# Optimization experiments

Hardware: AMD Instinct MI355X
Metric: run time of the kernel (lower is better)

Reference implementation:

```python
import jax, jax.numpy as jnp
import numpy as np

EPS = 1e-5
DIM, QK, PDIM = 448, 16, 96

def _bn(y, w, b, rm, rv):
    # inference-mode BatchNorm2d over channel axis 1
    scale = (w / jnp.sqrt(rv + EPS))[None, :, None, None]
    return (y - rm[None, :, None, None]) * scale + b[None, :, None, None]

def setup_inputs() -> dict:
    key = jax.random.key(0)
    ks = jax.random.split(key, 13)
    B, H, W = 64, 32, 32
    return {
        "x": jax.random.normal(ks[0], (B, DIM, H, W), jnp.float32),
        "gn_w": jax.random.uniform(ks[1], (PDIM,), jnp.float32, 0.5, 1.5),
        "gn_b": 0.02 * jax.random.normal(ks[2], (PDIM,), jnp.float32),
        "qkv_w": jax.random.normal(ks[3], (2 * QK + PDIM, PDIM), jnp.float32) * (PDIM ** -0.5),
        "qkv_bn_w": jax.random.uniform(ks[4], (2 * QK + PDIM,), jnp.float32, 0.5, 1.5),
        "qkv_bn_b": 0.02 * jax.random.normal(ks[5], (2 * QK + PDIM,), jnp.float32),
        "qkv_bn_rm": 0.02 * jax.random.normal(ks[6], (2 * QK + PDIM,), jnp.float32),
        "qkv_bn_rv": jax.random.uniform(ks[7], (2 * QK + PDIM,), jnp.float32, 0.5, 1.5),
        "proj_w": jax.random.normal(ks[8], (DIM, DIM), jnp.float32) * (DIM ** -0.5),
        "proj_bn_w": jax.random.uniform(ks[9], (DIM,), jnp.float32, 0.5, 1.5),
        "proj_bn_b": 0.02 * jax.random.normal(ks[10], (DIM,), jnp.float32),
        "proj_bn_rm": 0.02 * jax.random.normal(ks[11], (DIM,), jnp.float32),
        "proj_bn_rv": jax.random.uniform(ks[12], (DIM,), jnp.float32, 0.5, 1.5),
    }

def reference(x, gn_w, gn_b, qkv_w, qkv_bn_w, qkv_bn_b, qkv_bn_rm, qkv_bn_rv,
              proj_w, proj_bn_w, proj_bn_b, proj_bn_rm, proj_bn_rv):
    B, C, H, W = x.shape
    scale = QK ** -0.5
    x1, x2 = x[:, :PDIM], x[:, PDIM:]
    # GroupNorm with num_groups=1: normalize over (C,H,W) per sample
    mu = jnp.mean(x1, axis=(1, 2, 3), keepdims=True)
    var = jnp.var(x1, axis=(1, 2, 3), keepdims=True)
    x1n = (x1 - mu) * jax.lax.rsqrt(var + EPS)
    x1n = x1n * gn_w[None, :, None, None] + gn_b[None, :, None, None]
    # 1x1 conv (no bias) + BN
    qkv = jnp.einsum('bchw,oc->bohw', x1n, qkv_w)
    qkv = _bn(qkv, qkv_bn_w, qkv_bn_b, qkv_bn_rm, qkv_bn_rv)
    q, k, v = qkv[:, :QK], qkv[:, QK:2 * QK], qkv[:, 2 * QK:]
    N = H * W
    q = q.reshape(B, QK, N); k = k.reshape(B, QK, N); v = v.reshape(B, PDIM, N)
    attn = jnp.einsum('bcn,bcm->bnm', q, k) * scale          # [B,N,N]
    attn = jax.nn.softmax(attn, axis=-1)
    x1o = jnp.einsum('bcm,bnm->bcn', v, attn).reshape(B, PDIM, H, W)
    y = jnp.concatenate([x1o, x2], axis=1)
    y = jax.nn.relu(y)
    y = jnp.einsum('bchw,oc->bohw', y, proj_w)
    return _bn(y, proj_bn_w, proj_bn_b, proj_bn_rm, proj_bn_rv)
```

## Files before the change

### kernel.cpp

```cpp
#include <hip/hip_runtime.h>
#include <hip/hip_bf16.h>

#define EPS 1e-5f

constexpr int BB   = 64;
constexpr int CDIM = 448;
constexpr int PD   = 96;
constexpr int QKD  = 16;
constexpr int QO   = 128;
constexpr int NPix = 1024;
constexpr int NCH  = 14;

constexpr size_t WS_MU  = 0;
constexpr size_t WS_RS  = 64;
constexpr size_t WS_QSC = 128;
constexpr size_t WS_QBI = 256;
constexpr size_t WS_PSC = 384;
constexpr size_t WS_PBI = 832;
constexpr size_t WS_WG  = 1280;
constexpr size_t WS_SWG = 13568;
constexpr size_t WS_WB  = 13696;
constexpr size_t WS_WGT = 13824;
constexpr size_t WS_WGH = 26112;
constexpr size_t WS_YB  = 32768;
constexpr size_t WS_W16 = WS_YB + (size_t)BB*NPix*CDIM/2;
constexpr size_t WS_QT  = WS_W16 + (size_t)512*CDIM/2;
constexpr size_t WS_KT  = WS_QT + (size_t)BB*NPix*32/2;
constexpr size_t WS_VB  = WS_KT + (size_t)BB*NPix*32/2;

typedef __attribute__((ext_vector_type(8))) short short8;
typedef __attribute__((ext_vector_type(8))) _Float16 half8;
typedef __attribute__((ext_vector_type(4))) float f32x4;

__device__ __forceinline__ unsigned short f2bf(float v) {
  __hip_bfloat16 h = __float2bfloat16(v);
  return *reinterpret_cast<unsigned short*>(&h);
}
__device__ __forceinline__ unsigned short f2h(float v) {
  _Float16 h = (_Float16)v;
  return *reinterpret_cast<unsigned short*>(&h);
}

typedef const __attribute__((address_space(1))) unsigned int* gp_t;
typedef __attribute__((address_space(3))) unsigned int* lp_t;
__device__ __forceinline__ void gload16(const void* g, void* l) {
  __builtin_amdgcn_global_load_lds((gp_t)g, (lp_t)l, 16, 0, 0);
}

constexpr int XT_BLOCKS = 11264;
constexpr int TAILB     = 209;
__global__ __launch_bounds__(256) void k_setup(
    const float* __restrict__ x,
    const float* __restrict__ gn_w, const float* __restrict__ gn_b,
    const float* __restrict__ qkv_w,
    const float* __restrict__ qbw, const float* __restrict__ qbb,
    const float* __restrict__ qbrm, const float* __restrict__ qbrv,
    const float* __restrict__ pw,
    const float* __restrict__ pbw, const float* __restrict__ pbb,
    const float* __restrict__ pbrm, const float* __restrict__ pbrv,
    float* __restrict__ ws, unsigned short* __restrict__ Wb,
    unsigned short* __restrict__ Ybc) {
  __shared__ float tile[32][65];
  float* red = &tile[0][0];
  int t = threadIdx.x;
  if (blockIdx.x >= TAILB) {
    int idx = blockIdx.x - TAILB;
    int nx = idx & 15, cy = (idx >> 4) % 11, b = idx / 176;
    int c0 = PD + cy * 32;
    int n0 = nx * 64;
#pragma unroll
    for (int i = 0; i < 2; ++i) {
      int k = t + i * 256;
      int c = k >> 4, q = k & 15;
      float4 v = reinterpret_cast<const float4*>(
                     x + ((size_t)b * CDIM + c0 + c) * NPix + n0)[q];
      *reinterpret_cast<float4*>(&tile[c][q * 4]) = v;
    }
    __syncthreads();
    int n = t >> 2, ch = t & 3;
    short8 o;
#pragma unroll
    for (int j = 0; j < 8; ++j)
      o[j] = (short)f2bf(fmaxf(tile[ch * 8 + j][n], 0.f));
    *reinterpret_cast<short8*>(
        &Ybc[(((size_t)b * NCH + 3 + cy) * NPix + n0 + n) * 32 + ch * 8]) = o;
    return;
  }
  int bid = blockIdx.x;
  if (bid < 64) {
    int b = bid;
    const float4* x4 = reinterpret_cast<const float4*>(x + (size_t)b * CDIM * NPix);
    float s = 0.f, ss = 0.f;
#pragma unroll 8
    for (int ii = 0; ii < PD * NPix / 4 / 256; ++ii) {
      float4 v = x4[t + ii * 256];
      s  += v.x + v.y + v.z + v.w;
      ss += v.x * v.x + v.y * v.y + v.z * v.z + v.w * v.w;
    }
#pragma unroll
    for (int o = 32; o > 0; o >>= 1) { s += __shfl_down(s, o); ss += __shfl_down(ss, o); }
    int wid = t >> 6;
    if ((t & 63) == 0) { red[wid] = s; red[4 + wid] = ss; }
    __syncthreads();
    if (t == 0) {
      float S  = red[0] + red[1] + red[2] + red[3];
      float SS = red[4] + red[5] + red[6] + red[7];
      const float inv_n = 1.f / (PD * NPix);
      float mu  = S * inv_n;
      float var = SS * inv_n - mu * mu;
      ws[WS_MU + b] = mu;
      ws[WS_RS + b] = rsqrtf(var + EPS);
    }
  } else if (bid < 96) {
    int o = (bid - 64) * 4 + (t >> 6);
    int lane = t & 63;
    unsigned short* Wgh = reinterpret_cast<unsigned short*>(ws + WS_WGH);
    float sw = 0.f, bb = 0.f;
    for (int c = lane; c < PD; c += 64) {
      float w  = qkv_w[o * PD + c];
      float wg = w * gn_w[c];
      Wgh[(size_t)o * PD + c] = f2h(wg);
      sw += wg;
      bb += w * gn_b[c];
    }
#pragma unroll
    for (int off = 32; off > 0; off >>= 1) {
      sw += __shfl_down(sw, off);
      bb += __shfl_down(bb, off);
    }
    if (lane == 0) {
      ws[WS_SWG + o] = sw;
      ws[WS_WB + o]  = bb;
      float sc = qbw[o] * rsqrtf(qbrv[o] + EPS);
      ws[WS_QSC + o] = sc;
      ws[WS_QBI + o] = qbb[o] - qbrm[o] * sc;
    }
  } else if (bid == 96) {
    for (int o = t; o < CDIM; o += 256) {
      float sc = pbw[o] * rsqrtf(pbrv[o] + EPS);
      ws[WS_PSC + o] = sc;
      ws[WS_PBI + o] = pbb[o] - pbrm[o] * sc;
    }
  } else {
    int idx = (bid - 97) * 256 + t;
    int row = idx / 56, sl = (idx % 56) * 8;
    short8 o = {};
    if (row < CDIM) {
      const float* src = pw + (size_t)row * CDIM + sl;
#pragma unroll
      for (int j = 0; j < 8; ++j) o[j] = (short)f2bf(src[j]);
    }
    *reinterpret_cast<short8*>(&Wb[(size_t)row * CDIM + sl]) = o;
  }
}

__global__ __launch_bounds__(256) void k_qkv2(const float* __restrict__ x,
                                              float* __restrict__ ws,
                                              unsigned short* __restrict__ qt,
                                              unsigned short* __restrict__ kt,
                                              unsigned short* __restrict__ vb) {
  __shared__ __align__(16) char smem[PD * 132 * 4];
  float*          xt = reinterpret_cast<float*>(smem);
  unsigned short* ld = reinterpret_cast<unsigned short*>(smem);

  int lin = blockIdx.x + 8 * blockIdx.y;
  int swz = (lin & 7) * 64 + (lin >> 3);
  int n0  = (swz & 7) * 128;
  int b   = swz >> 3;
  int t   = threadIdx.x;
  int lane = t & 63, w = t >> 6;
  int lo = lane & 15, hi = lane >> 4;

  const float4* xb4 = reinterpret_cast<const float4*>(x + (size_t)b * CDIM * NPix);
#pragma unroll
  for (int i = 0; i < 12; ++i) {
    int idx = t + i * 256;
    int row = idx >> 5, c4 = idx & 31;
    float4 v = xb4[row * (NPix / 4) + (n0 >> 2) + c4];
    *reinterpret_cast<float4*>(&xt[row * 132 + c4 * 4]) = v;
  }
  __syncthreads();

  const unsigned short* Wgh = reinterpret_cast<const unsigned short*>(ws + WS_WGH);
  f32x4 acc[8][2] = {{{}}};
#pragma unroll
  for (int kk = 0; kk < 3; ++kk) {
    half8 bfr[2];
#pragma unroll
    for (int nf = 0; nf < 2; ++nf) {
      int nr = w * 32 + nf * 16 + lo;
      half8 h;
#pragma unroll
      for (int j = 0; j < 8; ++j)
        h[j] = (_Float16)xt[(kk * 32 + hi * 8 + j) * 132 + nr];
      bfr[nf] = h;
    }
#pragma unroll
    for (int of = 0; of < 8; ++of) {
      half8 a = *reinterpret_cast<const half8*>(
          &Wgh[(size_t)(of * 16 + lo) * PD + kk * 32 + hi * 8]);
      acc[of][0] = __builtin_amdgcn_mfma_f32_16x16x32_f16(a, bfr[0], acc[of][0], 0, 0, 0);
      acc[of][1] = __builtin_amdgcn_mfma_f32_16x16x32_f16(a, bfr[1], acc[of][1], 0, 0, 0);
    }
  }
  float mu = ws[WS_MU + b], rs = ws[WS_RS + b];
  __syncthreads();
#pragma unroll
  for (int of = 0; of < 8; ++of) {
#pragma unroll
    for (int r = 0; r < 4; ++r) {
      int o = of * 16 + hi * 4 + r;
      float bias = ws[WS_WB + o] - rs * mu * ws[WS_SWG + o];
      float qs = ws[WS_QSC + o], qb = ws[WS_QBI + o];
      float postm = (o < QKD) ? 0.25f : 1.f;
#pragma unroll
      for (int nf = 0; nf < 2; ++nf) {
        int nl = w * 32 + nf * 16 + lo;
        float v = (qs * (rs * acc[of][nf][r] + bias) + qb) * postm;
        ld[o * 136 + nl] = f2h(v);
      }
    }
  }
  __syncthreads();
#pragma unroll
  for (int i = 0; i < 6; ++i) {
    int idx = t + i * 256;
    int row = idx >> 4, c8 = idx & 15;
    short8 v = *reinterpret_cast<const short8*>(&ld[(32 + row) * 136 + c8 * 8]);
    *reinterpret_cast<short8*>(&vb[((size_t)b * PD + row) * NPix + n0 + c8 * 8]) = v;
  }
#pragma unroll
  for (int i = 0; i < 4; ++i) {
    int idx = t + i * 256;
    int arr = idx >> 9;
    int rem = idx & 511;
    int n = rem >> 2, q4 = rem & 3;
    short8 o = {};
    if (q4 < 2) {
#pragma unroll
      for (int j = 0; j < 8; ++j)
        o[j] = (short)ld[(arr * 16 + q4 * 8 + j) * 136 + n];
    }
    unsigned short* dst = arr ? kt : qt;
    *reinterpret_cast<short8*>(&dst[((size_t)b * NPix + n0 + n) * 32 + q4 * 8]) = o;
  }
}

__global__ __launch_bounds__(512) void k_attn2(
    const unsigned short* __restrict__ qt,
    const unsigned short* __restrict__ kt,
    const unsigned short* __restrict__ vb,
    unsigned short* __restrict__ Ybc) {
  __shared__ __align__(16) unsigned short kt_s[128 * 40];
  __shared__ __align__(16) unsigned short vt_s[96 * 136];
  __shared__ __align__(16) unsigned short P_s[8 * 16 * 136];

  int lin = blockIdx.x + 8 * blockIdx.y;
  int swz = (lin & 7) * 64 + (lin >> 3);
  int n0  = (swz & 7) * 128;
  int b   = swz >> 3;
  int t  = threadIdx.x;
  int lane = t & 63, w = t >> 6;
  int lo = lane & 15, hi = lane >> 4;

  half8 q8 = *reinterpret_cast<const half8*>(
      &qt[((size_t)b * NPix + n0 + w * 16 + lo) * 32 + hi * 8]);

  const unsigned short* ktb = kt + (size_t)b * NPix * 32;
  const unsigned short* vbb = vb + (size_t)b * PD * NPix;

  f32x4 o[6] = {};
  float M = -1e30f, L = 0.f;
  f32x4 zero = {};

  for (int mt = 0; mt < 8; ++mt) {
    int m0 = mt * 128;
    int krow = t >> 2, kc4 = t & 3;
    float4 rk = *reinterpret_cast<const float4*>(&ktb[(size_t)(m0 + krow) * 32 + kc4 * 8]);
    float4 rv[3];
#pragma unroll
    for (int i = 0; i < 3; ++i) {
      int ci = t + 512 * i;
      int row = ci >> 4, c4 = ci & 15;
      rv[i] = *reinterpret_cast<const float4*>(&vbb[(size_t)row * NPix + m0 + c4 * 8]);
    }
    __syncthreads();
    *reinterpret_cast<float4*>(&kt_s[krow * 40 + kc4 * 8]) = rk;
#pragma unroll
    for (int i = 0; i < 3; ++i) {
      int ci = t + 512 * i;
      int row = ci >> 4, c4 = ci & 15;
      *reinterpret_cast<float4*>(&vt_s[row * 136 + c4 * 8]) = rv[i];
    }
    __syncthreads();

    f32x4 s[8];
    __builtin_amdgcn_s_setprio(1);
#pragma unroll
    for (int ss = 0; ss < 8; ++ss) {
      half8 a = *reinterpret_cast<const half8*>(&kt_s[(ss * 16 + lo) * 40 + hi * 8]);
      s[ss] = __builtin_amdgcn_mfma_f32_16x16x32_f16(a, q8, zero, 0, 0, 0);
    }
    __builtin_amdgcn_s_setprio(0);

    float tmax = s[0][0];
#pragma unroll
    for (int ss = 0; ss < 8; ++ss)
#pragma unroll
      for (int r = 0; r < 4; ++r) tmax = fmaxf(tmax, s[ss][r]);
    tmax = fmaxf(tmax, __shfl_xor(tmax, 16));
    tmax = fmaxf(tmax, __shfl_xor(tmax, 32));
    float newM = fmaxf(M, tmax);
    float fac = __expf(M - newM);
    M = newM;
    float psum = 0.f;
    unsigned pbase = (w * 16 + lo) * 136;
#pragma unroll
    for (int ss = 0; ss < 8; ++ss) {
      float p0 = __expf(s[ss][0] - M);
      float p1 = __expf(s[ss][1] - M);
      float p2 = __expf(s[ss][2] - M);
      float p3 = __expf(s[ss][3] - M);
      psum += (p0 + p1) + (p2 + p3);
      unsigned u01 = (unsigned)f2h(p0) | ((unsigned)f2h(p1) << 16);
      unsigned u23 = (unsigned)f2h(p2) | ((unsigned)f2h(p3) << 16);
      *reinterpret_cast<unsigned*>(&P_s[pbase + 16 * ss + 4 * hi])     = u01;
      *reinterpret_cast<unsigned*>(&P_s[pbase + 16 * ss + 4 * hi + 2]) = u23;
    }
    psum += __shfl_xor(psum, 16);
    psum += __shfl_xor(psum, 32);
    L = L * fac + psum;
#pragma unroll
    for (int cf = 0; cf < 6; ++cf)
#pragma unroll
      for (int r = 0; r < 4; ++r) o[cf][r] *= fac;
    asm volatile("s_waitcnt lgkmcnt(0)" ::: "memory");

    __builtin_amdgcn_s_setprio(1);
#pragma unroll
    for (int ks = 0; ks < 4; ++ks) {
      half8 pb = *reinterpret_cast<const half8*>(&P_s[pbase + ks * 32 + hi * 8]);
#pragma unroll
      for (int cf = 0; cf < 6; ++cf) {
        half8 va = *reinterpret_cast<const half8*>(&vt_s[(cf * 16 + lo) * 136 + ks * 32 + hi * 8]);
        o[cf] = __builtin_amdgcn_mfma_f32_16x16x32_f16(va, pb, o[cf], 0, 0, 0);
      }
    }
    __builtin_amdgcn_s_setprio(0);
  }

  float inv = 1.f / L;
  unsigned pbase = (w * 16 + lo) * 136;
#pragma unroll
  for (int cf = 0; cf < 6; ++cf) {
    float v0 = fmaxf(o[cf][0] * inv, 0.f);
    float v1 = fmaxf(o[cf][1] * inv, 0.f);
    float v2 = fmaxf(o[cf][2] * inv, 0.f);
    float v3 = fmaxf(o[cf][3] * inv, 0.f);
    unsigned u01 = (unsigned)f2bf(v0) | ((unsigned)f2bf(v1) << 16);
    unsigned u23 = (unsigned)f2bf(v2) | ((unsigned)f2bf(v3) << 16);
    *reinterpret_cast<unsigned*>(&P_s[pbase + cf * 16 + 4 * hi])     = u01;
    *reinterpret_cast<unsigned*>(&P_s[pbase + cf * 16 + 4 * hi + 2]) = u23;
  }
  asm volatile("s_waitcnt lgkmcnt(0)" ::: "memory");
#pragma unroll
  for (int j = 0; j < 3; ++j) {
    int k = lane + 64 * j;
    int n = k / 12, c8 = k % 12;
    short8 vv = *reinterpret_cast<const short8*>(&P_s[(w * 16 + n) * 136 + c8 * 8]);
    *reinterpret_cast<short8*>(
        &Ybc[(((size_t)b * NCH + (c8 >> 2)) * NPix + n0 + w * 16 + n) * 32
             + (c8 & 3) * 8]) = vv;
  }
}

__global__ __launch_bounds__(256) void k_projmm(
    const unsigned short* __restrict__ Wb,
    const unsigned short* __restrict__ Ybc,
    const float* __restrict__ ws,
    float* __restrict__ out) {
  __shared__ __align__(16) unsigned short At[3][128 * 32];
  int lin = blockIdx.x + 8 * (blockIdx.y + 4 * blockIdx.z);
  int swz = (lin & 7) * 256 + (lin >> 3);
  int m0  = (swz & 3) * 128;
  int n0  = ((swz >> 2) & 7) * 128;
  int b   = swz >> 5;
  int t  = threadIdx.x;
  int lane = t & 63, wid = t >> 6;
  int wm = wid >> 1, wn = wid & 1;
  int lo = lane & 15, hi = lane >> 4;

  const unsigned short* Arow = Wb + (size_t)m0 * CDIM;
  const unsigned short* Brow = Ybc + ((size_t)b * NCH * NPix + n0 + wn * 64) * 32;

  int chunk0 = wid * 128 + lane;
  int row0 = chunk0 >> 2, sl0 = (chunk0 & 3) ^ ((row0 >> 1) & 3);
  int chunk1 = chunk0 + 64;
  int row1 = chunk1 >> 2, sl1 = (chunk1 & 3) ^ ((row1 >> 1) & 3);

#define STAGE_A(bufi, s_)                                                      \
  do {                                                                         \
    gload16(Arow + (size_t)row0 * CDIM + (s_) * 32 + sl0 * 8,                  \
            &At[bufi][(wid * 128) * 8]);                                       \
    gload16(Arow + (size_t)row1 * CDIM + (s_) * 32 + sl1 * 8,                  \
            &At[bufi][(wid * 128 + 64) * 8]);                                  \
  } while (0)

#define LOADB(slot, s_)                                                        \
  do {                                                                         \
    _Pragma("unroll")                                                          \
    for (int f = 0; f < 4; ++f)                                                \
      bf[slot][f] = *reinterpret_cast<const short8*>(                          \
          &Brow[(size_t)(s_) * NPix * 32 + (f * 16 + lo) * 32 + hi * 8]);      \
  } while (0)

  short8 bf[2][4];
  f32x4 acc[4][4] = {{{}}};

  STAGE_A(0, 0);
  STAGE_A(1, 1);
  LOADB(0, 0);
  asm volatile("s_waitcnt vmcnt(6)" ::: "memory");
  __builtin_amdgcn_sched_barrier(0);
  __builtin_amdgcn_s_barrier();

#pragma unroll
  for (int s = 0; s < 14; ++s) {
    if (s + 2 <= 13) STAGE_A((s + 2) % 3, s + 2);
    if (s + 1 <= 13) LOADB((s + 1) & 1, s + 1);
    __builtin_amdgcn_sched_barrier(0);
    short8 af[4];
#pragma unroll
    for (int f = 0; f < 4; ++f) {
      int ar = wm * 64 + f * 16 + lo;
      int as = hi ^ ((ar >> 1) & 3);
      af[f] = *reinterpret_cast<const short8*>(&At[s % 3][ar * 32 + as * 8]);
    }
    asm volatile("s_waitcnt lgkmcnt(0)" ::: "memory");
    __builtin_amdgcn_sched_barrier(0);
#pragma unroll
    for (int i = 0; i < 4; ++i)
#pragma unroll
      for (int j = 0; j < 4; ++j)
        acc[i][j] = __builtin_amdgcn_mfma_f32_16x16x32_bf16(
            af[i], bf[s & 1][j], acc[i][j], 0, 0, 0);
    if (s < 13) {
      if (s <= 11) asm volatile("s_waitcnt vmcnt(6)" ::: "memory");
      else         asm volatile("s_waitcnt vmcnt(4)" ::: "memory");
      __builtin_amdgcn_sched_barrier(0);
      __builtin_amdgcn_s_barrier();
    }
  }
#undef STAGE_A
#undef LOADB

  int col = lane & 15, rq = lane >> 4;
#pragma unroll
  for (int i = 0; i < 4; ++i) {
    int ob = m0 + wm * 64 + i * 16 + rq * 4;
#pragma unroll
    for (int r = 0; r < 4; ++r) {
      int o = ob + r;
      if (o < CDIM) {
        float ps = ws[WS_PSC + o], pb = ws[WS_PBI + o];
        size_t base = ((size_t)b * CDIM + o) * NPix + n0 + wn * 64 + col;
#pragma unroll
        for (int j = 0; j < 4; ++j)
          out[base + j * 16] = ps * acc[i][j][r] + pb;
      }
    }
  }
}

extern "C" void kernel_launch(void* const* d_in, const int* in_sizes, int n_in,
                              void* d_out, int out_size, void* d_ws, size_t ws_size,
                              hipStream_t stream) {
  const float* x      = (const float*)d_in[0];
  const float* gn_w   = (const float*)d_in[1];
  const float* gn_b   = (const float*)d_in[2];
  const float* qkv_w  = (const float*)d_in[3];
  const float* qbw    = (const float*)d_in[4];
  const float* qbb    = (const float*)d_in[5];
  const float* qbrm   = (const float*)d_in[6];
  const float* qbrv   = (const float*)d_in[7];
  const float* pw     = (const float*)d_in[8];
  const float* pbw    = (const float*)d_in[9];
  const float* pbb    = (const float*)d_in[10];
  const float* pbrm   = (const float*)d_in[11];
  const float* pbrv   = (const float*)d_in[12];
  float* out = (float*)d_out;
  float* ws  = (float*)d_ws;
  unsigned short* Ybc = (unsigned short*)(ws + WS_YB);
  unsigned short* Wb  = (unsigned short*)(ws + WS_W16);
  unsigned short* qt  = (unsigned short*)(ws + WS_QT);
  unsigned short* kt  = (unsigned short*)(ws + WS_KT);
  unsigned short* vb  = (unsigned short*)(ws + WS_VB);

  k_setup<<<TAILB + XT_BLOCKS, 256, 0, stream>>>(
      x, gn_w, gn_b, qkv_w, qbw, qbb, qbrm, qbrv,
      pw, pbw, pbb, pbrm, pbrv, ws, Wb, Ybc);
  k_qkv2<<<dim3(8, BB), 256, 0, stream>>>(x, ws, qt, kt, vb);
  k_attn2<<<dim3(8, BB), 512, 0, stream>>>(qt, kt, vb, Ybc);
  k_projmm<<<dim3(8, 4, BB), 256, 0, stream>>>(Wb, Ybc, ws, out);
}
```

Baseline: 138.7 us.

## Redistribute x2 ReLU/transpose work into qkv and attn kernels; deepen projmm K-step

The ReLU + bf16 transpose of the pass-through channels (x2) moves out of the setup kernel and is split across extra blocks appended to the qkv and attention kernels. Batches 0-31 go to qkv, batches 32-63 go to attention, so this bandwidth-bound work can fill CUs alongside the compute-heavy blocks. Separately, the projection GEMM doubles its K tile from 32 to 64 per stage, using an 8-way XOR swizzle, 7 iterations instead of 14, and s_setprio around the MFMA bursts. This halves the number of barriers per tile at the cost of more LDS and registers, which may lower occupancy.

```diff
diff --git a/kernel.cpp b/kernel.cpp
--- a/kernel.cpp
+++ b/kernel.cpp
@@ -47,8 +47,7 @@
   __builtin_amdgcn_global_load_lds((gp_t)g, (lp_t)l, 16, 0, 0);
 }
 
-constexpr int XT_BLOCKS = 11264;
-constexpr int TAILB     = 209;
+constexpr int TAILB = 209;
 __global__ __launch_bounds__(256) void k_setup(
     const float* __restrict__ x,
     const float* __restrict__ gn_w, const float* __restrict__ gn_b,
@@ -58,34 +57,9 @@
     const float* __restrict__ pw,
     const float* __restrict__ pbw, const float* __restrict__ pbb,
     const float* __restrict__ pbrm, const float* __restrict__ pbrv,
-    float* __restrict__ ws, unsigned short* __restrict__ Wb,
-    unsigned short* __restrict__ Ybc) {
-  __shared__ float tile[32][65];
-  float* red = &tile[0][0];
+    float* __restrict__ ws, unsigned short* __restrict__ Wb) {
+  __shared__ float red[8];
   int t = threadIdx.x;
-  if (blockIdx.x >= TAILB) {
-    int idx = blockIdx.x - TAILB;
-    int nx = idx & 15, cy = (idx >> 4) % 11, b = idx / 176;
-    int c0 = PD + cy * 32;
-    int n0 = nx * 64;
-#pragma unroll
-    for (int i = 0; i < 2; ++i) {
-      int k = t + i * 256;
-      int c = k >> 4, q = k & 15;
-      float4 v = reinterpret_cast<const float4*>(
-                     x + ((size_t)b * CDIM + c0 + c) * NPix + n0)[q];
-      *reinterpret_cast<float4*>(&tile[c][q * 4]) = v;
-    }
-    __syncthreads();
-    int n = t >> 2, ch = t & 3;
-    short8 o;
-#pragma unroll
-    for (int j = 0; j < 8; ++j)
-      o[j] = (short)f2bf(fmaxf(tile[ch * 8 + j][n], 0.f));
-    *reinterpret_cast<short8*>(
-        &Ybc[(((size_t)b * NCH + 3 + cy) * NPix + n0 + n) * 32 + ch * 8]) = o;
-    return;
-  }
   int bid = blockIdx.x;
   if (bid < 64) {
     int b = bid;
@@ -158,16 +132,42 @@
                                               float* __restrict__ ws,
                                               unsigned short* __restrict__ qt,
                                               unsigned short* __restrict__ kt,
-                                              unsigned short* __restrict__ vb) {
+                                              unsigned short* __restrict__ vb,
+                                              unsigned short* __restrict__ Ybc) {
   __shared__ __align__(16) char smem[PD * 132 * 4];
   float*          xt = reinterpret_cast<float*>(smem);
   unsigned short* ld = reinterpret_cast<unsigned short*>(smem);
-
-  int lin = blockIdx.x + 8 * blockIdx.y;
+  int t = threadIdx.x;
+
+  if (blockIdx.x >= 512) {
+    int idx = (int)blockIdx.x - 512;
+    int nx = idx & 15, cy = (idx >> 4) % 11, bb = idx / 176;
+    int c0 = PD + cy * 32;
+    int n0x = nx * 64;
+    float* txt = reinterpret_cast<float*>(smem);
+#pragma unroll
+    for (int i = 0; i < 2; ++i) {
+      int k = t + i * 256;
+      int c = k >> 4, q = k & 15;
+      float4 v = reinterpret_cast<const float4*>(
+                     x + ((size_t)bb * CDIM + c0 + c) * NPix + n0x)[q];
+      *reinterpret_cast<float4*>(&txt[c * 65 + q * 4]) = v;
+    }
+    __syncthreads();
+    int n = t >> 2, ch = t & 3;
+    short8 o;
+#pragma unroll
+    for (int j = 0; j < 8; ++j)
+      o[j] = (short)f2bf(fmaxf(txt[(ch * 8 + j) * 65 + n], 0.f));
+    *reinterpret_cast<short8*>(
+        &Ybc[(((size_t)bb * NCH + 3 + cy) * NPix + n0x + n) * 32 + ch * 8]) = o;
+    return;
+  }
+
+  int lin = blockIdx.x;
   int swz = (lin & 7) * 64 + (lin >> 3);
   int n0  = (swz & 7) * 128;
   int b   = swz >> 3;
-  int t   = threadIdx.x;
   int lane = t & 63, w = t >> 6;
   int lo = lane & 15, hi = lane >> 4;
 
@@ -247,6 +247,7 @@
 }
 
 __global__ __launch_bounds__(512) void k_attn2(
+    const float* __restrict__ x,
     const unsigned short* __restrict__ qt,
     const unsigned short* __restrict__ kt,
     const unsigned short* __restrict__ vb,
@@ -254,12 +255,37 @@
   __shared__ __align__(16) unsigned short kt_s[128 * 40];
   __shared__ __align__(16) unsigned short vt_s[96 * 136];
   __shared__ __align__(16) unsigned short P_s[8 * 16 * 136];
-
-  int lin = blockIdx.x + 8 * blockIdx.y;
+  int t = threadIdx.x;
+
+  if (blockIdx.x >= 512) {
+    int idx = (int)blockIdx.x - 512;
+    int nx = idx & 7, cy = (idx >> 3) % 11, bb = 32 + idx / 88;
+    int c0 = PD + cy * 32;
+    int n0x = nx * 128;
+    float* txt = reinterpret_cast<float*>(P_s);
+#pragma unroll
+    for (int i = 0; i < 2; ++i) {
+      int k = t + i * 512;
+      int c = k >> 5, q = k & 31;
+      float4 v = reinterpret_cast<const float4*>(
+                     x + ((size_t)bb * CDIM + c0 + c) * NPix + n0x)[q];
+      *reinterpret_cast<float4*>(&txt[c * 130 + q * 4]) = v;
+    }
+    __syncthreads();
+    int n = t >> 2, ch = t & 3;
+    short8 o;
+#pragma unroll
+    for (int j = 0; j < 8; ++j)
+      o[j] = (short)f2bf(fmaxf(txt[(ch * 8 + j) * 130 + n], 0.f));
+    *reinterpret_cast<short8*>(
+        &Ybc[(((size_t)bb * NCH + 3 + cy) * NPix + n0x + n) * 32 + ch * 8]) = o;
+    return;
+  }
+
+  int lin = blockIdx.x;
   int swz = (lin & 7) * 64 + (lin >> 3);
   int n0  = (swz & 7) * 128;
   int b   = swz >> 3;
-  int t  = threadIdx.x;
   int lane = t & 63, w = t >> 6;
   int lo = lane & 15, hi = lane >> 4;
 
@@ -379,7 +405,7 @@
     const unsigned short* __restrict__ Ybc,
     const float* __restrict__ ws,
     float* __restrict__ out) {
-  __shared__ __align__(16) unsigned short At[3][128 * 32];
+  __shared__ __align__(16) unsigned short At[3][128 * 64];
   int lin = blockIdx.x + 8 * (blockIdx.y + 4 * blockIdx.z);
   int swz = (lin & 7) * 256 + (lin >> 3);
   int m0  = (swz & 3) * 128;
@@ -393,62 +419,76 @@
   const unsigned short* Arow = Wb + (size_t)m0 * CDIM;
   const unsigned short* Brow = Ybc + ((size_t)b * NCH * NPix + n0 + wn * 64) * 32;
 
-  int chunk0 = wid * 128 + lane;
-  int row0 = chunk0 >> 2, sl0 = (chunk0 & 3) ^ ((row0 >> 1) & 3);
-  int chunk1 = chunk0 + 64;
-  int row1 = chunk1 >> 2, sl1 = (chunk1 & 3) ^ ((row1 >> 1) & 3);
+  int rowi[4], lsl[4];
+#pragma unroll
+  for (int i = 0; i < 4; ++i) {
+    int c = wid * 256 + i * 64 + lane;
+    rowi[i] = c >> 3;
+    lsl[i]  = (c & 7) ^ (rowi[i] & 7);
+  }
 
 #define STAGE_A(bufi, s_)                                                      \
   do {                                                                         \
-    gload16(Arow + (size_t)row0 * CDIM + (s_) * 32 + sl0 * 8,                  \
-            &At[bufi][(wid * 128) * 8]);                                       \
-    gload16(Arow + (size_t)row1 * CDIM + (s_) * 32 + sl1 * 8,                  \
-            &At[bufi][(wid * 128 + 64) * 8]);                                  \
+    _Pragma("unroll")                                                          \
+    for (int i = 0; i < 4; ++i)                                                \
+      gload16(Arow + (size_t)rowi[i] * CDIM + (s_) * 64 + lsl[i] * 8,          \
+              &At[bufi][(wid * 256 + i * 64) * 8]);                            \
   } while (0)
 
-#define LOADB(slot, s_)                                                        \
+#define LOADB(par, s_)                                                         \
   do {                                                                         \
     _Pragma("unroll")                                                          \
-    for (int f = 0; f < 4; ++f)                                                \
-      bf[slot][f] = *reinterpret_cast<const short8*>(                          \
-          &Brow[(size_t)(s_) * NPix * 32 + (f * 16 + lo) * 32 + hi * 8]);      \
+    for (int k0 = 0; k0 < 2; ++k0)                                             \
+      _Pragma("unroll")                                                        \
+      for (int f = 0; f < 4; ++f)                                              \
+        bf[par][k0][f] = *reinterpret_cast<const short8*>(                     \
+            &Brow[(size_t)(2 * (s_) + k0) * NPix * 32 + (f * 16 + lo) * 32 +   \
+                  hi * 8]);                                                    \
   } while (0)
 
-  short8 bf[2][4];
+  short8 bf[2][2][4];
   f32x4 acc[4][4] = {{{}}};
 
   STAGE_A(0, 0);
   STAGE_A(1, 1);
   LOADB(0, 0);
-  asm volatile("s_waitcnt vmcnt(6)" ::: "memory");
+  asm volatile("s_waitcnt vmcnt(12)" ::: "memory");
   __builtin_amdgcn_sched_barrier(0);
   __builtin_amdgcn_s_barrier();
-
-#pragma unroll
-  for (int s = 0; s < 14; ++s) {
-    if (s + 2 <= 13) STAGE_A((s + 2) % 3, s + 2);
-    if (s + 1 <= 13) LOADB((s + 1) & 1, s + 1);
+  __builtin_amdgcn_sched_barrier(0);
+
+#pragma unroll
+  for (int s = 0; s < 7; ++s) {
+    if (s + 2 <= 6) STAGE_A((s + 2) % 3, s + 2);
+    if (s + 1 <= 6) LOADB((s + 1) & 1, s + 1);
     __builtin_amdgcn_sched_barrier(0);
-    short8 af[4];
+    short8 af0[4], af1[4];
 #pragma unroll
     for (int f = 0; f < 4; ++f) {
       int ar = wm * 64 + f * 16 + lo;
-      int as = hi ^ ((ar >> 1) & 3);
-      af[f] = *reinterpret_cast<const short8*>(&At[s % 3][ar * 32 + as * 8]);
-    }
-    asm volatile("s_waitcnt lgkmcnt(0)" ::: "memory");
-    __builtin_amdgcn_sched_barrier(0);
+      int p0 = hi ^ (ar & 7);
+      int p1 = (4 + hi) ^ (ar & 7);
+      af0[f] = *reinterpret_cast<const short8*>(&At[s % 3][ar * 64 + p0 * 8]);
+      af1[f] = *reinterpret_cast<const short8*>(&At[s % 3][ar * 64 + p1 * 8]);
+    }
+    __builtin_amdgcn_s_setprio(1);
 #pragma unroll
     for (int i = 0; i < 4; ++i)
 #pragma unroll
       for (int j = 0; j < 4; ++j)
         acc[i][j] = __builtin_amdgcn_mfma_f32_16x16x32_bf16(
-            af[i], bf[s & 1][j], acc[i][j], 0, 0, 0);
-    if (s < 13) {
-      if (s <= 11) asm volatile("s_waitcnt vmcnt(6)" ::: "memory");
-      else         asm volatile("s_waitcnt vmcnt(4)" ::: "memory");
+            af0[i], bf[s & 1][0][j], acc[i][j], 0, 0, 0);
+#pragma unroll
+    for (int i = 0; i < 4; ++i)
+#pragma unroll
+      for (int j = 0; j < 4; ++j)
+        acc[i][j] = __builtin_amdgcn_mfma_f32_16x16x32_bf16(
+            af1[i], bf[s & 1][1][j], acc[i][j], 0, 0, 0);
+    __builtin_amdgcn_s_setprio(0);
+    if (s < 6) {
       __builtin_amdgcn_sched_barrier(0);
       __builtin_amdgcn_s_barrier();
+      __builtin_amdgcn_sched_barrier(0);
     }
   }
 #undef STAGE_A
@@ -496,10 +536,10 @@
   unsigned short* kt  = (unsigned short*)(ws + WS_KT);
   unsigned short* vb  = (unsigned short*)(ws + WS_VB);
 
-  k_setup<<<TAILB + XT_BLOCKS, 256, 0, stream>>>(
+  k_setup<<<TAILB, 256, 0, stream>>>(
       x, gn_w, gn_b, qkv_w, qbw, qbb, qbrm, qbrv,
-      pw, pbw, pbb, pbrm, pbrv, ws, Wb, Ybc);
-  k_qkv2<<<dim3(8, BB), 256, 0, stream>>>(x, ws, qt, kt, vb);
-  k_attn2<<<dim3(8, BB), 512, 0, stream>>>(qt, kt, vb, Ybc);
+      pw, pbw, pbb, pbrm, pbrv, ws, Wb);
+  k_qkv2<<<512 + 5632, 256, 0, stream>>>(x, ws, qt, kt, vb, Ybc);
+  k_attn2<<<512 + 2816, 512, 0, stream>>>(x, qt, kt, vb, Ybc);
   k_projmm<<<dim3(8, 4, BB), 256, 0, stream>>>(Wb, Ybc, ws, out);
 }
```

New measurement: 143.7 us. 3.6% more time.
